# Kernel optimization log

Measured on AMD Instinct MI355X. Metric: run time of the kernel, lower is better.

## Reference

```python
import jax, jax.numpy as jnp
import numpy as np

EPS = 1e-12  # torch F.normalize default eps

def _l2_normalize(x):
    # F.normalize(x, dim=1): x / max(||x||_2, eps), per row
    n = jnp.linalg.norm(x, axis=1, keepdims=True)
    return x / jnp.maximum(n, EPS)

def setup_inputs() -> dict:
    key = jax.random.key(0)
    ks = jax.random.split(key, 7)
    B, D = 8192, 4096
    s = 1.0 / np.sqrt(D)  # keep activations well-scaled like nn.Linear init
    return {
        "x":  jax.random.normal(ks[0], (B, D), dtype=jnp.float32),
        "W0": jax.random.normal(ks[1], (D, D), dtype=jnp.float32) * s,
        "b0": jax.random.normal(ks[2], (D,),   dtype=jnp.float32) * s,
        "W1": jax.random.normal(ks[3], (D, D), dtype=jnp.float32) * s,
        "b1": jax.random.normal(ks[4], (D,),   dtype=jnp.float32) * s,
        "W2": jax.random.normal(ks[5], (D, D), dtype=jnp.float32) * s,
        "b2": jax.random.normal(ks[6], (D,),   dtype=jnp.float32) * s,
    }

def reference(x, W0, b0, W1, b1, W2, b2):
    # per layer: out = relu(Linear(l2_normalize(x, dim=1))); collect all layer outputs
    params = [(W0, b0), (W1, b1), (W2, b2)]
    outs = []
    h = x
    for W, b in params:
        hn = _l2_normalize(h)
        # nn.Linear stores weight as [out, in]: y = hn @ W.T + b
        h = jax.nn.relu(jnp.einsum('bi,oi->bo', hn, W) + b)
        outs.append(h)
    return tuple(outs)
```

## Files before the change

kernel.cpp:

```cpp
#include <hip/hip_runtime.h>
#include <hip/hip_bf16.h>


#define NROWS 8192
#define DIM   4096

typedef __bf16 bf16x8 __attribute__((ext_vector_type(8)));
typedef float  f32x4  __attribute__((ext_vector_type(4)));

__device__ static inline short f2bf(float f) {
  __hip_bfloat16 h = __float2bfloat16(f);
  return __builtin_bit_cast(short, h);
}

#define BARRIER() do { asm volatile("" ::: "memory"); \
                       __builtin_amdgcn_s_barrier();  \
                       asm volatile("" ::: "memory"); } while (0)
#define GATE()   do { asm volatile("s_waitcnt lgkmcnt(0)" ::: "memory"); \
                      __builtin_amdgcn_sched_barrier(0); } while (0)

__global__ __launch_bounds__(512, 2)
void gemm256_bias_relu(const short* __restrict__ A,
                       const short* __restrict__ Bw,
                       const float* __restrict__ bias,
                       float* __restrict__ C,
                       int M, int N, int K)
{
  __shared__ short lds[4][16384];

  int bid = blockIdx.x;
  const int nwg = gridDim.x;
  if ((nwg & 7) == 0) { const int cpx = nwg >> 3; bid = (bid & 7) * cpx + (bid >> 3); }
  const int nbn  = N >> 8;
  const int brow = (bid / nbn) << 8;
  const int bcol = (bid % nbn) << 8;

  const int lane = threadIdx.x & 63;
  const int wid  = __builtin_amdgcn_readfirstlane(threadIdx.x >> 6);
  const int wr   = wid >> 2;
  const int wc   = wid & 3;

  float bv[4];
#pragma unroll
  for (int j = 0; j < 4; ++j)
    bv[j] = bias[bcol + wc * 64 + j * 16 + (lane & 15)];

  f32x4 acc[8][4] = {};

  const size_t rowK = (size_t)K * 2;
  char* const  ldsB = (char*)&lds[0][0];

  const int r8  = lane >> 3;
  const int kcs = (lane & 7) ^ r8;
  const char* AgL = (const char*)A  + (size_t)(brow + r8) * rowK + (size_t)kcs * 16;
  const char* BgL = (const char*)Bw + (size_t)(bcol + r8) * rowK + (size_t)kcs * 16;
  int rbo[4], rbb[4];
#pragma unroll
  for (int i = 0; i < 4; ++i) {
    const int rb = wid * 8 + i * 64;
    rbo[i] = rb * (int)rowK;
    rbb[i] = rb * 128;
  }

  auto stage_half = [&](int parity, int op, int h, int tile) {
    const char* gp = (op ? BgL : AgL) + ((size_t)tile << 7);
    char* lb = ldsB + (parity * 2 + op) * 32768;
#pragma unroll
    for (int s = 0; s < 2; ++s) {
      const int idx = h * 2 + s;
      __builtin_amdgcn_global_load_lds(
          (const __attribute__((address_space(1))) void*)(gp + rbo[idx]),
          (__attribute__((address_space(3))) void*)(lb + rbb[idx]), 16, 0, 0);
    }
  };

  const int l15  = lane & 15;
  const int xlo  = ((lane >> 4) ^ (lane & 3)) * 16;
  const int b2   = (lane >> 2) & 1;
  const int k64[2] = { b2 << 6, (1 - b2) << 6 };
  const int abase = (wr * 128 + l15) * 128 + xlo;
  const int bbase = (wc * 64  + l15) * 128 + xlo;

  const int NT = K >> 6;

  bf16x8 aX[4][2], aY[4][2], bF[4][2];

#define LOAD_FRAG(DST, PTR, BASE, I0)                                        \
  _Pragma("unroll")                                                          \
  for (int ii = 0; ii < 4; ++ii)                                             \
    _Pragma("unroll")                                                        \
    for (int ks = 0; ks < 2; ++ks)                                           \
      DST[ii][ks] = *reinterpret_cast<const bf16x8*>(                        \
          (PTR) + (BASE) + ((I0) + ii) * 2048 + k64[ks]);

#define MFMA16(I0, AF)                                                       \
  _Pragma("unroll")                                                          \
  for (int ks = 0; ks < 2; ++ks)                                             \
    _Pragma("unroll")                                                        \
    for (int ii = 0; ii < 4; ++ii)                                           \
      _Pragma("unroll")                                                      \
      for (int j = 0; j < 4; ++j)                                            \
        acc[(I0) + ii][j] = __builtin_amdgcn_mfma_f32_16x16x32_bf16(         \
            AF[ii][ks], bF[j][ks], acc[(I0) + ii][j], 0, 0, 0);

  stage_half(0, 0, 0, 0); stage_half(0, 0, 1, 0);
  stage_half(0, 1, 0, 0); stage_half(0, 1, 1, 0);
  if (NT > 1) { stage_half(1, 1, 0, 1); stage_half(1, 1, 1, 1); }
  if (NT > 1) asm volatile("s_waitcnt vmcnt(4)" ::: "memory");
  else        asm volatile("s_waitcnt vmcnt(0)" ::: "memory");
  BARRIER();
  LOAD_FRAG(aX, ldsB, abase, 0)

  for (int t = 0; t < NT; ++t) {
    const int cur = t & 1, nxt = cur ^ 1;
    const char* At = ldsB + (cur * 2 + 0) * 32768;
    const char* Bt = ldsB + (cur * 2 + 1) * 32768;
    const char* An = ldsB + (nxt * 2 + 0) * 32768;

    if (t + 1 < NT) { stage_half(nxt, 0, 0, t + 1); stage_half(nxt, 0, 1, t + 1); }
    LOAD_FRAG(bF, Bt, bbase, 0)
    BARRIER();
    GATE();
    LOAD_FRAG(aY, At, abase, 4)
    __builtin_amdgcn_s_setprio(1);
    MFMA16(0, aX)
    __builtin_amdgcn_s_setprio(0);

    asm volatile("s_waitcnt vmcnt(0)" ::: "memory");
    BARRIER();
    GATE();
    if (t + 2 < NT) { stage_half(cur, 1, 0, t + 2); stage_half(cur, 1, 1, t + 2); }
    if (t + 1 < NT) { LOAD_FRAG(aX, An, abase, 0) }
    __builtin_amdgcn_s_setprio(1);
    MFMA16(4, aY)
    __builtin_amdgcn_s_setprio(0);
  }
#undef MFMA16
#undef LOAD_FRAG

#pragma unroll
  for (int i = 0; i < 8; ++i) {
    const int rbase = brow + wr * 128 + i * 16 + ((lane >> 4) << 2);
#pragma unroll
    for (int j = 0; j < 4; ++j) {
      const int col = bcol + wc * 64 + j * 16 + (lane & 15);
#pragma unroll
      for (int r = 0; r < 4; ++r) {
        const float v = acc[i][j][r] + bv[j];
        C[(size_t)(rbase + r) * N + col] = v > 0.f ? v : 0.f;
      }
    }
  }
}

__global__ __launch_bounds__(256)
void rownorm_bf16(const float* __restrict__ in, short* __restrict__ out)
{
  const int row = blockIdx.x;
  const int t0  = threadIdx.x;
  const float4* inr = (const float4*)(in + (size_t)row * DIM);

  float4 v[4];
  float ss = 0.f;
#pragma unroll
  for (int t = 0; t < 4; ++t) {
    v[t] = inr[t0 + t * 256];
    ss += v[t].x * v[t].x + v[t].y * v[t].y + v[t].z * v[t].z + v[t].w * v[t].w;
  }
#pragma unroll
  for (int off = 32; off > 0; off >>= 1)
    ss += __shfl_down(ss, off, 64);

  __shared__ float wss[4];
  if ((t0 & 63) == 0) wss[t0 >> 6] = ss;
  __syncthreads();
  const float tot   = wss[0] + wss[1] + wss[2] + wss[3];
  const float scale = 1.f / fmaxf(sqrtf(tot), 1e-12f);

  short4* outr = (short4*)(out + (size_t)row * DIM);
#pragma unroll
  for (int t = 0; t < 4; ++t) {
    short4 o;
    o.x = f2bf(v[t].x * scale);
    o.y = f2bf(v[t].y * scale);
    o.z = f2bf(v[t].z * scale);
    o.w = f2bf(v[t].w * scale);
    outr[t0 + t * 256] = o;
  }
}

__global__ __launch_bounds__(256)
void cast_bf16(const float* __restrict__ in, short* __restrict__ out, int n4)
{
  int i = blockIdx.x * 256 + threadIdx.x;
  const int stride = gridDim.x * 256;
  for (; i < n4; i += stride) {
    const float4 v = ((const float4*)in)[i];
    short4 o;
    o.x = f2bf(v.x);
    o.y = f2bf(v.y);
    o.z = f2bf(v.z);
    o.w = f2bf(v.w);
    ((short4*)out)[i] = o;
  }
}

extern "C" void kernel_launch(void* const* d_in, const int* in_sizes, int n_in,
                              void* d_out, int out_size, void* d_ws, size_t ws_size,
                              hipStream_t stream) {
  const float* x = (const float*)d_in[0];
  const float* W[3]    = { (const float*)d_in[1], (const float*)d_in[3], (const float*)d_in[5] };
  const float* bias[3] = { (const float*)d_in[2], (const float*)d_in[4], (const float*)d_in[6] };
  float* out = (float*)d_out;

  short* hn = (short*)d_ws;
  short* Wb = (short*)((char*)d_ws + (size_t)NROWS * DIM * 2);

  const size_t layer_elems = (size_t)NROWS * DIM;
  const float* hin = x;

  for (int L = 0; L < 3; ++L) {
    cast_bf16<<<2048, 256, 0, stream>>>(W[L], Wb, DIM * DIM / 4);
    rownorm_bf16<<<NROWS, 256, 0, stream>>>(hin, hn);
    gemm256_bias_relu<<<(NROWS / 256) * (DIM / 256), 512, 0, stream>>>(
        hn, Wb, bias[L], out + (size_t)L * layer_elems, NROWS, DIM, DIM);
    hin = out + (size_t)L * layer_elems;
  }
}
```

Baseline: 779.2 us.

## Restructure GEMM main loop into four quadrant phases with finer-grained prefetch

Splits each K-tile iteration of the 256x256 bf16 GEMM into four MFMA quadrants (rows 0-3/4-7 by cols 0-1/2-3). LDS fragment reads and global->LDS staging are interleaved between the quadrants, and both A and B of the next tile are prefetched. The goal is to hide LDS read and global load latency more evenly behind MFMA work and keep the matrix cores busy. It adds more barriers per iteration and changes the vmcnt wait counts, so a wrong count or extra sync overhead could hurt or break correctness. The bias load is also moved after the loop to ease register pressure.

```diff
diff --git a/kernel.cpp b/kernel.cpp
--- a/kernel.cpp
+++ b/kernel.cpp
@@ -17,6 +17,8 @@
                        __builtin_amdgcn_s_barrier();  \
                        asm volatile("" ::: "memory"); } while (0)
 #define GATE()   do { asm volatile("s_waitcnt lgkmcnt(0)" ::: "memory"); \
+                      __builtin_amdgcn_sched_barrier(0); } while (0)
+#define VMW(N)   do { asm volatile("s_waitcnt vmcnt(" #N ")" ::: "memory"); \
                       __builtin_amdgcn_sched_barrier(0); } while (0)
 
 __global__ __launch_bounds__(512, 2)
@@ -40,11 +42,6 @@
   const int wr   = wid >> 2;
   const int wc   = wid & 3;
 
-  float bv[4];
-#pragma unroll
-  for (int j = 0; j < 4; ++j)
-    bv[j] = bias[bcol + wc * 64 + j * 16 + (lane & 15)];
-
   f32x4 acc[8][4] = {};
 
   const size_t rowK = (size_t)K * 2;
@@ -83,61 +80,90 @@
 
   const int NT = K >> 6;
 
-  bf16x8 aX[4][2], aY[4][2], bF[4][2];
-
-#define LOAD_FRAG(DST, PTR, BASE, I0)                                        \
+  bf16x8 a03[4][2], a47[4][2], bF[4][2];
+
+#define LOAD_A4(DST, PTR, I0)                                                \
   _Pragma("unroll")                                                          \
   for (int ii = 0; ii < 4; ++ii)                                             \
     _Pragma("unroll")                                                        \
     for (int ks = 0; ks < 2; ++ks)                                           \
       DST[ii][ks] = *reinterpret_cast<const bf16x8*>(                        \
-          (PTR) + (BASE) + ((I0) + ii) * 2048 + k64[ks]);
-
-#define MFMA16(I0, AF)                                                       \
+          (PTR) + abase + ((I0) + ii) * 2048 + k64[ks]);
+
+#define LOAD_B2(PTR, J0)                                                     \
+  _Pragma("unroll")                                                          \
+  for (int jj = 0; jj < 2; ++jj)                                             \
+    _Pragma("unroll")                                                        \
+    for (int ks = 0; ks < 2; ++ks)                                           \
+      bF[(J0) + jj][ks] = *reinterpret_cast<const bf16x8*>(                  \
+          (PTR) + bbase + ((J0) + jj) * 2048 + k64[ks]);
+
+#define MFMAQ(I0, J0, AF)                                                    \
   _Pragma("unroll")                                                          \
   for (int ks = 0; ks < 2; ++ks)                                             \
     _Pragma("unroll")                                                        \
     for (int ii = 0; ii < 4; ++ii)                                           \
       _Pragma("unroll")                                                      \
-      for (int j = 0; j < 4; ++j)                                            \
-        acc[(I0) + ii][j] = __builtin_amdgcn_mfma_f32_16x16x32_bf16(         \
-            AF[ii][ks], bF[j][ks], acc[(I0) + ii][j], 0, 0, 0);
+      for (int jj = 0; jj < 2; ++jj)                                         \
+        acc[(I0) + ii][(J0) + jj] = __builtin_amdgcn_mfma_f32_16x16x32_bf16( \
+            AF[ii][ks], bF[(J0) + jj][ks], acc[(I0) + ii][(J0) + jj], 0, 0, 0);
 
   stage_half(0, 0, 0, 0); stage_half(0, 0, 1, 0);
   stage_half(0, 1, 0, 0); stage_half(0, 1, 1, 0);
-  if (NT > 1) { stage_half(1, 1, 0, 1); stage_half(1, 1, 1, 1); }
-  if (NT > 1) asm volatile("s_waitcnt vmcnt(4)" ::: "memory");
-  else        asm volatile("s_waitcnt vmcnt(0)" ::: "memory");
+  if (NT > 1) { VMW(4); }
+  if (NT > 1) { stage_half(1, 0, 0, 1); stage_half(1, 0, 1, 1);
+                stage_half(1, 1, 0, 1); }
+  if (NT > 1) { VMW(6); } else { VMW(0); }
   BARRIER();
-  LOAD_FRAG(aX, ldsB, abase, 0)
 
   for (int t = 0; t < NT; ++t) {
     const int cur = t & 1, nxt = cur ^ 1;
     const char* At = ldsB + (cur * 2 + 0) * 32768;
     const char* Bt = ldsB + (cur * 2 + 1) * 32768;
-    const char* An = ldsB + (nxt * 2 + 0) * 32768;
-
-    if (t + 1 < NT) { stage_half(nxt, 0, 0, t + 1); stage_half(nxt, 0, 1, t + 1); }
-    LOAD_FRAG(bF, Bt, bbase, 0)
+
+    LOAD_A4(a03, At, 0)
+    LOAD_B2(Bt, 0)
+    if (t + 1 < NT) stage_half(nxt, 1, 1, t + 1);
     BARRIER();
     GATE();
-    LOAD_FRAG(aY, At, abase, 4)
-    __builtin_amdgcn_s_setprio(1);
-    MFMA16(0, aX)
-    __builtin_amdgcn_s_setprio(0);
-
-    asm volatile("s_waitcnt vmcnt(0)" ::: "memory");
+    __builtin_amdgcn_s_setprio(1);
+    MFMAQ(0, 0, a03)
+    __builtin_amdgcn_s_setprio(0);
+    BARRIER();
+
+    LOAD_A4(a47, At, 4)
     BARRIER();
     GATE();
-    if (t + 2 < NT) { stage_half(cur, 1, 0, t + 2); stage_half(cur, 1, 1, t + 2); }
-    if (t + 1 < NT) { LOAD_FRAG(aX, An, abase, 0) }
-    __builtin_amdgcn_s_setprio(1);
-    MFMA16(4, aY)
-    __builtin_amdgcn_s_setprio(0);
-  }
-#undef MFMA16
-#undef LOAD_FRAG
-
+    __builtin_amdgcn_s_setprio(1);
+    MFMAQ(4, 0, a47)
+    __builtin_amdgcn_s_setprio(0);
+    BARRIER();
+
+    LOAD_B2(Bt, 2)
+    if (t + 2 < NT) { stage_half(cur, 0, 0, t + 2); stage_half(cur, 0, 1, t + 2); }
+    BARRIER();
+    GATE();
+    __builtin_amdgcn_s_setprio(1);
+    MFMAQ(4, 2, a47)
+    __builtin_amdgcn_s_setprio(0);
+    BARRIER();
+
+    if (t + 2 < NT) stage_half(cur, 1, 0, t + 2);
+    if (t >= NT - 2) { VMW(0); } else { VMW(6); }
+    BARRIER();
+    __builtin_amdgcn_s_setprio(1);
+    MFMAQ(0, 2, a03)
+    __builtin_amdgcn_s_setprio(0);
+    BARRIER();
+  }
+#undef MFMAQ
+#undef LOAD_A4
+#undef LOAD_B2
+
+  float bv[4];
+#pragma unroll
+  for (int j = 0; j < 4; ++j)
+    bv[j] = bias[bcol + wc * 64 + j * 16 + (lane & 15)];
 #pragma unroll
   for (int i = 0; i < 8; ++i) {
     const int rbase = brow + wr * 128 + i * 16 + ((lane >> 4) << 2);
```

Measured after the change: 823.7 us. 1.06x slower.
